# Kernel tuning notes

Hardware: AMD Instinct MI355X
Metric: run time of the kernel (lower is better)

Reference implementation:

```python
import jax, jax.numpy as jnp
import numpy as np

NUM_HEADS = 12
REDUCTION = 4
ALPHA_SPIKING = 0.5
ALPHA_ORIG = 0.5
K_BIAS = 1.0
BN_EPS = 1e-5


def dual_spike(x):
    # DualThresholdSelfregulatingIntegrateAction, T=1, dt=1: ternary spike at +/-1 thresholds
    return jnp.where(x >= 1.0, 1.0, jnp.where(x <= -1.0, -1.0, 0.0)).astype(x.dtype)


def setup_inputs() -> dict:
    key = jax.random.key(0)
    ks = jax.random.split(key, 12)
    B, S, Dm, H = 8, 512, 768, NUM_HEADS
    R = H // REDUCTION
    sc = 1.0 / np.sqrt(Dm).astype(np.float32)
    hidden_states = jax.random.normal(ks[0], (B, S, Dm), jnp.float32)
    attention_mask = jnp.zeros((B, 1, 1, S), jnp.float32)
    Wq = jax.random.normal(ks[1], (Dm, Dm), jnp.float32) * sc
    bq = jnp.zeros((Dm,), jnp.float32)
    Wk = jax.random.normal(ks[2], (Dm, Dm), jnp.float32) * sc
    bk = jnp.zeros((Dm,), jnp.float32)
    Wv = jax.random.normal(ks[3], (Dm, Dm), jnp.float32) * sc
    bv = jnp.zeros((Dm,), jnp.float32)
    # inline 1x1 convs of linesnn_mcz (bias=False), stored as [out_ch, in_ch]
    conv1_w = jax.random.normal(ks[4], (R, H), jnp.float32) * (1.0 / np.sqrt(H).astype(np.float32))
    bn_gamma = jnp.ones((R,), jnp.float32)
    bn_beta = jnp.zeros((R,), jnp.float32)
    convh_w = jax.random.normal(ks[5], (H, R), jnp.float32) * (1.0 / np.sqrt(R).astype(np.float32))
    convw_w = jax.random.normal(ks[6], (H, R), jnp.float32) * (1.0 / np.sqrt(R).astype(np.float32))
    return dict(hidden_states=hidden_states, attention_mask=attention_mask,
                Wq=Wq, bq=bq, Wk=Wk, bk=bk, Wv=Wv, bv=bv,
                conv1_w=conv1_w, bn_gamma=bn_gamma, bn_beta=bn_beta,
                convh_w=convh_w, convw_w=convw_w)


def _forward(hidden_states, attention_mask, Wq, bq, Wk, bk, Wv, bv,
             conv1_w, bn_gamma, bn_beta, convh_w, convw_w):
    B, S, Dm = hidden_states.shape
    H = NUM_HEADS
    D = Dm // H

    q_lin = hidden_states @ Wq + bq
    k_lin = hidden_states @ Wk + bk
    v_lin = jax.lax.stop_gradient(hidden_states @ Wv + bv)  # value is .detach()'d

    q = dual_spike(q_lin)                                   # spiking Q
    k = ALPHA_SPIKING * dual_spike(k_lin) + ALPHA_ORIG * k_lin

    def heads(x):  # [B,S,Dm] -> [B,H,S,D]
        return x.reshape(B, S, H, D).transpose(0, 2, 1, 3)

    q, k, v = heads(q), heads(k), heads(v_lin)

    scores = jnp.einsum('bhqd,bhkd->bhqk', q, k) / np.sqrt(D).astype(np.float32)

    # ---- select_linesnn / linesnn_mcz bias branch (on pre-mask scores) ----
    # spiking_activation_v then IF(v_th=1): spike = 1 where ternary spike == 1
    t = (dual_spike(scores) >= 1.0).astype(scores.dtype)    # [B,H,S,S]
    xh = t.mean(axis=3)                                     # mean over width  -> [B,H,S]
    xw = t.mean(axis=2)                                     # mean over height -> [B,H,S]
    cat = jnp.concatenate([xh, xw], axis=2)                 # [B,H,2S]
    y = jnp.einsum('rc,bcn->brn', conv1_w, cat)             # 1x1 conv H->R
    mu = y.mean(axis=(0, 2), keepdims=True)                 # BatchNorm (training stats)
    var = ((y - mu) ** 2).mean(axis=(0, 2), keepdims=True)
    y = (y - mu) * jax.lax.rsqrt(var + BN_EPS)
    y = y * bn_gamma[None, :, None] + bn_beta[None, :, None]
    y = jax.nn.relu(y)
    yh, yw = y[:, :, :S], y[:, :, S:]                       # split([h,w])
    s_h = jax.nn.sigmoid(jnp.einsum('hr,brs->bhs', convh_w, yh))  # [B,H,S]
    s_w = jax.nn.sigmoid(jnp.einsum('hr,brs->bhs', convw_w, yw))  # [B,H,S]
    bias = t * s_h[:, :, :, None] * s_w[:, :, None, :]      # [B,H,S,S]

    scores = scores + attention_mask + K_BIAS * bias
    probs = jax.nn.softmax(scores, axis=-1)                 # dropout p=0 (inference)
    ctx = jnp.einsum('bhqk,bhkd->bhqd', probs, v)
    return ctx.transpose(0, 2, 1, 3).reshape(B, S, Dm)


def reference(hidden_states, attention_mask, Wq, bq, Wk, bk, Wv, bv,
              conv1_w, bn_gamma, bn_beta, convh_w, convw_w):
    return _forward(hidden_states, attention_mask, Wq, bq, Wk, bk, Wv, bv,
                    conv1_w, bn_gamma, bn_beta, convh_w, convw_w)
```

## Files before the change

### kernel.cpp

```cpp
#include <hip/hip_runtime.h>
#include <math.h>

#define B_   8
#define S_   512
#define DM_  768
#define H_   12
#define D_   64
#define BH_  96
#define M_   4096

typedef _Float16 f16x8 __attribute__((ext_vector_type(8)));
typedef float    f32x4 __attribute__((ext_vector_type(4)));

__device__ __forceinline__ float dual_spike(float x) {
    return x >= 1.0f ? 1.0f : (x <= -1.0f ? -1.0f : 0.0f);
}

__device__ __forceinline__ void gload_lds16(const void* g, void* l) {
    __builtin_amdgcn_global_load_lds(
        (const __attribute__((address_space(1))) unsigned int*)g,
        (__attribute__((address_space(3))) unsigned int*)l, 16, 0, 0);
}

__device__ __forceinline__ f32x4 qk_dot(const f16x8* qa, const f16x8* kh, const f16x8* kl) {
    f32x4 acc = (f32x4){0.f, 0.f, 0.f, 0.f};
    acc = __builtin_amdgcn_mfma_f32_16x16x32_f16(qa[0], kh[0], acc, 0, 0, 0);
    acc = __builtin_amdgcn_mfma_f32_16x16x32_f16(qa[0], kl[0], acc, 0, 0, 0);
    acc = __builtin_amdgcn_mfma_f32_16x16x32_f16(qa[1], kh[1], acc, 0, 0, 0);
    acc = __builtin_amdgcn_mfma_f32_16x16x32_f16(qa[1], kl[1], acc, 0, 0, 0);
    return acc;
}

__global__ __launch_bounds__(256) void prep_x(
    const float* __restrict__ X, _Float16* __restrict__ Xh, _Float16* __restrict__ Xl)
{
    int wid  = blockIdx.x * 4 + (threadIdx.x >> 6);
    int lane = threadIdx.x & 63;
    int fm = wid & 255, kc = wid >> 8;
    int row = fm * 16 + (lane & 15);
    int col = kc * 32 + (lane >> 4) * 8;
    const float4* p = reinterpret_cast<const float4*>(&X[row * DM_ + col]);
    float4 x0 = p[0], x1 = p[1];
    float xs[8] = {x0.x, x0.y, x0.z, x0.w, x1.x, x1.y, x1.z, x1.w};
    f16x8 hi, lo;
    #pragma unroll
    for (int j = 0; j < 8; ++j) {
        float v = xs[j] * 256.0f;
        _Float16 h = (_Float16)v;
        hi[j] = h;
        lo[j] = (_Float16)(v - (float)h);
    }
    size_t out = ((size_t)wid * 64 + lane) * 8;
    *reinterpret_cast<f16x8*>(&Xh[out]) = hi;
    *reinterpret_cast<f16x8*>(&Xl[out]) = lo;
}

__global__ __launch_bounds__(256) void prep_w(
    const float* __restrict__ Wq, const float* __restrict__ Wk, const float* __restrict__ Wv,
    _Float16* __restrict__ Wth, _Float16* __restrict__ Wtl)
{
    int wid  = blockIdx.x * 4 + (threadIdx.x >> 6);
    int lane = threadIdx.x & 63;
    int fn = wid % 48, kc = (wid / 48) % 24, which = wid / 1152;
    const float* __restrict__ W = which == 0 ? Wq : (which == 1 ? Wk : Wv);
    int c = lane & 15, g = lane >> 4;
    int ncol = fn * 16 + c;
    int krow = kc * 32 + g * 8;
    f16x8 hi, lo;
    #pragma unroll
    for (int j = 0; j < 8; ++j) {
        float v = W[(krow + j) * DM_ + ncol] * 256.0f;
        _Float16 h = (_Float16)v;
        hi[j] = h;
        lo[j] = (_Float16)(v - (float)h);
    }
    size_t out = ((size_t)wid * 64 + lane) * 8;
    *reinterpret_cast<f16x8*>(&Wth[out]) = hi;
    *reinterpret_cast<f16x8*>(&Wtl[out]) = lo;
}

__global__ __launch_bounds__(512, 4) void qkv_mfma(
    const _Float16* __restrict__ Xh, const _Float16* __restrict__ Xl,
    const _Float16* __restrict__ Wth, const _Float16* __restrict__ Wtl,
    const float* __restrict__ X,
    const float* __restrict__ Wq, const float* __restrict__ bq,
    const float* __restrict__ Wk, const float* __restrict__ bk,
    const float* __restrict__ Wv, const float* __restrict__ bv,
    float* __restrict__ q, float* __restrict__ k, float* __restrict__ v)
{
    const int orig = blockIdx.x;
    const int xcd = orig & 7, idx = orig >> 3;
    const int epoch = idx >> 5, sub = idx & 31;
    const int mw = xcd * 12 + epoch * 4 + (sub >> 3);
    const int which = mw / 32, mb = mw % 32;
    const int nb = sub & 7;

    const float* __restrict__ bias = which == 0 ? bq : (which == 1 ? bk : bv);
    float* __restrict__ out        = which == 0 ? q  : (which == 1 ? k  : v);

    __shared__ __align__(16) _Float16 lds[2][14336];

    const int tid = threadIdx.x;
    const int wave = tid >> 6, lane = tid & 63;
    const int wm = wave >> 1, wn = wave & 1;
    const int l15 = lane & 15, g = lane >> 4;

    auto stage = [&](int kc, int bsel) {
        #pragma unroll
        for (int c = 0; c < 4; ++c) {
            int u = wave * 4 + c;
            if (u < 28) {
                const _Float16* src;
                if (u < 8)       src = Xh  + (size_t)(kc * 256 + mb * 8 + u) * 512;
                else if (u < 16) src = Xl  + (size_t)(kc * 256 + mb * 8 + (u - 8)) * 512;
                else if (u < 22) src = Wth + (size_t)((which * 24 + kc) * 48 + nb * 6 + (u - 16)) * 512;
                else             src = Wtl + (size_t)((which * 24 + kc) * 48 + nb * 6 + (u - 22)) * 512;
                gload_lds16(src + lane * 8, &lds[bsel][u * 512]);
            }
        }
    };

    f32x4 acc[2][3];
    #pragma unroll
    for (int i = 0; i < 2; ++i)
        #pragma unroll
        for (int j = 0; j < 3; ++j) acc[i][j] = (f32x4){0.f, 0.f, 0.f, 0.f};

    stage(0, 0);
    __syncthreads();
    int cur = 0;

    for (int kc = 0; kc < 24; ++kc) {
        if (kc + 1 < 24) stage(kc + 1, cur ^ 1);
        const _Float16* Bf = lds[cur];
        f16x8 ah[2], al[2], bh[3], bl[3];
        #pragma unroll
        for (int f = 0; f < 2; ++f) {
            ah[f] = *reinterpret_cast<const f16x8*>(&Bf[(wm * 2 + f) * 512 + lane * 8]);
            al[f] = *reinterpret_cast<const f16x8*>(&Bf[4096 + (wm * 2 + f) * 512 + lane * 8]);
        }
        #pragma unroll
        for (int fb = 0; fb < 3; ++fb) {
            bh[fb] = *reinterpret_cast<const f16x8*>(&Bf[8192 + (wn * 3 + fb) * 512 + lane * 8]);
            bl[fb] = *reinterpret_cast<const f16x8*>(&Bf[11264 + (wn * 3 + fb) * 512 + lane * 8]);
        }
        __builtin_amdgcn_s_setprio(1);
        #pragma unroll
        for (int i = 0; i < 2; ++i)
            #pragma unroll
            for (int j = 0; j < 3; ++j) {
                acc[i][j] = __builtin_amdgcn_mfma_f32_16x16x32_f16(ah[i], bh[j], acc[i][j], 0, 0, 0);
                acc[i][j] = __builtin_amdgcn_mfma_f32_16x16x32_f16(ah[i], bl[j], acc[i][j], 0, 0, 0);
                acc[i][j] = __builtin_amdgcn_mfma_f32_16x16x32_f16(al[i], bh[j], acc[i][j], 0, 0, 0);
            }
        __builtin_amdgcn_s_setprio(0);
        __syncthreads();
        cur ^= 1;
    }

    const float* __restrict__ Worig = which == 0 ? Wq : (which == 1 ? Wk : Wv);

    #pragma unroll
    for (int i = 0; i < 2; ++i) {
        #pragma unroll
        for (int j = 0; j < 3; ++j) {
            int n = nb * 96 + wn * 48 + j * 16 + l15;
            int h = n >> 6, d = n & 63;
            float bn = bias[n];
            #pragma unroll
            for (int r = 0; r < 4; ++r) {
                int m = mb * 128 + wm * 32 + i * 16 + g * 4 + r;
                float val = acc[i][j][r] * (1.0f / 65536.0f) + bn;
                if (which < 2) {
                    bool need = fabsf(fabsf(val) - 1.0f) < 1e-4f;
                    unsigned long long msk = __ballot(need);
                    while (msk) {
                        int L = (int)__builtin_ctzll(msk);
                        msk &= msk - 1;
                        int Lm = mb * 128 + wm * 32 + i * 16 + (L >> 4) * 4 + r;
                        int Ln = nb * 96 + wn * 48 + j * 16 + (L & 15);
                        const float* xr = X + (size_t)Lm * DM_;
                        const float* wc = Worig + Ln;
                        float xs[12], wsv[12];
                        #pragma unroll
                        for (int t = 0; t < 12; ++t) {
                            int e = t * 64 + lane;
                            xs[t]  = xr[e];
                            wsv[t] = wc[(size_t)e * DM_];
                        }
                        float part = 0.0f;
                        #pragma unroll
                        for (int t = 0; t < 12; ++t) part = fmaf(xs[t], wsv[t], part);
                        part += __shfl_xor(part, 1);
                        part += __shfl_xor(part, 2);
                        part += __shfl_xor(part, 4);
                        part += __shfl_xor(part, 8);
                        part += __shfl_xor(part, 16);
                        part += __shfl_xor(part, 32);
                        if (lane == L) val = part + bn;
                    }
                }
                if (which == 0)      val = dual_spike(val);
                else if (which == 1) val = 0.5f * dual_spike(val) + 0.5f * val;
                int b = m >> 9, s = m & 511;
                out[(((b * H_ + h) * S_) + s) * D_ + d] = val;
            }
        }
    }
}

__global__ __launch_bounds__(256) void prep_qkv(
    const float* __restrict__ q, const float* __restrict__ k, const float* __restrict__ v,
    _Float16* __restrict__ Qf, _Float16* __restrict__ Kfh, _Float16* __restrict__ Kfl,
    _Float16* __restrict__ Vfh, _Float16* __restrict__ Vfl)
{
    int lane = threadIdx.x & 63;
    int l15 = lane & 15, g = lane >> 4;
    if (blockIdx.x < 1536) {
        int wid  = blockIdx.x * 4 + (threadIdx.x >> 6);
        int dc = wid & 1, s16 = (wid >> 1) & 31, bh = wid >> 6;
        int s = s16 * 16 + l15;
        int d0 = dc * 32 + g * 8;
        const float* qp = &q[((size_t)bh * S_ + s) * D_ + d0];
        const float* kp = &k[((size_t)bh * S_ + s) * D_ + d0];
        f16x8 qv, kh, kl;
        #pragma unroll
        for (int j = 0; j < 8; ++j) {
            qv[j] = (_Float16)qp[j];
            float val = kp[j] * 256.0f;
            _Float16 h = (_Float16)val;
            kh[j] = h;
            kl[j] = (_Float16)(val - (float)h);
        }
        size_t o = (size_t)wid * 512 + lane * 8;
        *reinterpret_cast<f16x8*>(&Qf[o])  = qv;
        *reinterpret_cast<f16x8*>(&Kfh[o]) = kh;
        *reinterpret_cast<f16x8*>(&Kfl[o]) = kl;
    } else {
        int wid  = (blockIdx.x - 1536) * 4 + (threadIdx.x >> 6);
        int d16 = wid & 3, kc = (wid >> 2) & 15, bh = wid >> 6;
        int d = d16 * 16 + l15;
        int k0 = kc * 32 + g * 8;
        const float* vp = &v[((size_t)bh * S_ + k0) * D_ + d];
        f16x8 hi, lo;
        #pragma unroll
        for (int j = 0; j < 8; ++j) {
            float val = vp[j * D_];
            _Float16 h = (_Float16)val;
            hi[j] = h;
            lo[j] = (_Float16)(val - (float)h);
        }
        size_t o = (size_t)wid * 512 + lane * 8;
        *reinterpret_cast<f16x8*>(&Vfh[o]) = hi;
        *reinterpret_cast<f16x8*>(&Vfl[o]) = lo;
    }
}

__global__ __launch_bounds__(256) void score_sums(
    const _Float16* __restrict__ Qf, const _Float16* __restrict__ Kfh,
    const _Float16* __restrict__ Kfl,
    float* __restrict__ xh, float* __restrict__ xw)
{
    const int orig = blockIdx.x;
    const int xcd = orig & 7, idx = orig >> 3;
    const int bh = xcd * 12 + idx / 8, qt = idx & 7;
    const int tid = threadIdx.x, wave = tid >> 6, lane = tid & 63;
    const int l15 = lane & 15, g = lane >> 4;

    __shared__ float rowred[4][64];

    f16x8 qa[4][2];
    #pragma unroll
    for (int sf = 0; sf < 4; ++sf) {
        const _Float16* qb = Qf + (size_t)((bh * 32 + qt * 4 + sf) * 2) * 512 + lane * 8;
        qa[sf][0] = *reinterpret_cast<const f16x8*>(qb);
        qa[sf][1] = *reinterpret_cast<const f16x8*>(qb + 512);
    }
    float rowc[4][4];
    #pragma unroll
    for (int sf = 0; sf < 4; ++sf)
        #pragma unroll
        for (int r = 0; r < 4; ++r) rowc[sf][r] = 0.0f;

    for (int sc8 = 0; sc8 < 8; ++sc8) {
        int scol16 = sc8 * 4 + wave;
        const _Float16* kbh = Kfh + (size_t)((bh * 32 + scol16) * 2) * 512 + lane * 8;
        const _Float16* kbl = Kfl + (size_t)((bh * 32 + scol16) * 2) * 512 + lane * 8;
        f16x8 kh[2] = {*reinterpret_cast<const f16x8*>(kbh),
                       *reinterpret_cast<const f16x8*>(kbh + 512)};
        f16x8 kl[2] = {*reinterpret_cast<const f16x8*>(kbl),
                       *reinterpret_cast<const f16x8*>(kbl + 512)};
        float csum = 0.0f;
        #pragma unroll
        for (int sf = 0; sf < 4; ++sf) {
            f32x4 acc = qk_dot(qa[sf], kh, kl);
            #pragma unroll
            for (int r = 0; r < 4; ++r) {
                float t1 = acc[r] >= 2048.0f ? 1.0f : 0.0f;
                rowc[sf][r] += t1;
                csum += t1;
            }
        }
        csum += __shfl_xor(csum, 16);
        csum += __shfl_xor(csum, 32);
        if (g == 0) atomicAdd(&xw[bh * S_ + scol16 * 16 + l15], csum);
    }
    #pragma unroll
    for (int sf = 0; sf < 4; ++sf)
        #pragma unroll
        for (int r = 0; r < 4; ++r) {
            float sv = rowc[sf][r];
            sv += __shfl_xor(sv, 1); sv += __shfl_xor(sv, 2);
            sv += __shfl_xor(sv, 4); sv += __shfl_xor(sv, 8);
            if (l15 == 0) rowred[wave][sf * 16 + g * 4 + r] = sv;
        }
    __syncthreads();
    if (tid < 64) {
        float sv = rowred[0][tid] + rowred[1][tid] + rowred[2][tid] + rowred[3][tid];
        xh[bh * S_ + qt * 64 + tid] = sv;
    }
}

__global__ __launch_bounds__(256) void small_a(
    const float* __restrict__ xh, const float* __restrict__ xw,
    const float* __restrict__ c1w,
    float* __restrict__ y, float* __restrict__ stats_part)
{
    const int tid = threadIdx.x;
    const int br = blockIdx.x;
    const int r = br % 3, b = br / 3;
    __shared__ float c1s[12];
    __shared__ float red[256], red2[256];
    if (tid < 12) c1s[tid] = c1w[r * 12 + tid];
    __syncthreads();

    float psum = 0.0f, psq = 0.0f;
    for (int n = tid; n < 1024; n += 256) {
        float acc = 0.0f;
        #pragma unroll
        for (int h = 0; h < 12; ++h) {
            float cv = (n < 512) ? xh[(b * H_ + h) * S_ + n]
                                 : xw[(b * H_ + h) * S_ + (n - 512)];
            acc = fmaf(c1s[h], cv * (1.0f / 512.0f), acc);
        }
        y[br * 1024 + n] = acc;
        psum += acc;
        psq = fmaf(acc, acc, psq);
    }
    red[tid] = psum; red2[tid] = psq;
    __syncthreads();
    for (int o = 128; o > 0; o >>= 1) {
        if (tid < o) { red[tid] += red[tid + o]; red2[tid] += red2[tid + o]; }
        __syncthreads();
    }
    if (tid == 0) {
        stats_part[br * 2 + 0] = red[0];
        stats_part[br * 2 + 1] = red2[0];
    }
}

__global__ __launch_bounds__(512) void small_b(
    const float* __restrict__ y, const float* __restrict__ stats_part,
    const float* __restrict__ gamma, const float* __restrict__ beta,
    const float* __restrict__ chw, const float* __restrict__ cww,
    float* __restrict__ s_h, float* __restrict__ s_w)
{
    int e = blockIdx.x * 512 + threadIdx.x;
    int s = e & 511; int bh = e >> 9; int h = bh % H_; int b = bh / H_;
    float ah = 0.0f, aw = 0.0f;
    #pragma unroll
    for (int r = 0; r < 3; ++r) {
        float su = 0.0f, sq = 0.0f;
        #pragma unroll
        for (int bb = 0; bb < 8; ++bb) {
            su += stats_part[(bb * 3 + r) * 2 + 0];
            sq += stats_part[(bb * 3 + r) * 2 + 1];
        }
        float mu = su * (1.0f / 8192.0f);
        float var = sq * (1.0f / 8192.0f) - mu * mu;
        float rs = rsqrtf(var + 1e-5f);
        int yb = (b * 3 + r) << 10;
        float yh = fmaxf((y[yb + s]       - mu) * rs * gamma[r] + beta[r], 0.0f);
        float yw = fmaxf((y[yb + 512 + s] - mu) * rs * gamma[r] + beta[r], 0.0f);
        ah = fmaf(chw[h * 3 + r], yh, ah);
        aw = fmaf(cww[h * 3 + r], yw, aw);
    }
    s_h[e] = 1.0f / (1.0f + expf(-ah));
    s_w[e] = 1.0f / (1.0f + expf(-aw));
}

__global__ __launch_bounds__(256) void attn_pv(
    const _Float16* __restrict__ Qf, const _Float16* __restrict__ Kfh,
    const _Float16* __restrict__ Kfl,
    const _Float16* __restrict__ Vfh, const _Float16* __restrict__ Vfl,
    const float* __restrict__ mask, const float* __restrict__ s_h,
    const float* __restrict__ s_w, float* __restrict__ out)
{
    __shared__ __align__(16) _Float16 Kst[2][4096];
    __shared__ __align__(16) _Float16 Vst[2][4096];
    __shared__ __align__(16) float P_lds[64][68];

    const int orig = blockIdx.x;
    const int xcd = orig & 7, idx = orig >> 3;
    const int bh = xcd * 12 + idx / 8, qt = idx & 7;
    const int b = bh / H_, h = bh % H_;
    const int q0 = qt * 64;
    const int tid = threadIdx.x, wave = tid >> 6, lane = tid & 63;
    const int l15 = lane & 15, g = lane >> 4;
    const int rl = wave * 16 + g * 4;

    const _Float16* qb = Qf + (size_t)((bh * 32 + qt * 4 + wave) * 2) * 512 + lane * 8;
    f16x8 qa[2] = {*reinterpret_cast<const f16x8*>(qb),
                   *reinterpret_cast<const f16x8*>(qb + 512)};

    float shq[4];
    #pragma unroll
    for (int r = 0; r < 4; ++r) shq[r] = s_h[bh * S_ + q0 + rl + r];

    auto stageK = [&](int kt) {
        const _Float16* sh_ = Kfh + (size_t)((bh * 32 + kt * 4) * 2) * 512;
        const _Float16* sl_ = Kfl + (size_t)((bh * 32 + kt * 4) * 2) * 512;
        #pragma unroll
        for (int c = 0; c < 2; ++c) {
            int u = (c * 4 + wave) * 512;
            gload_lds16(&sh_[u + lane * 8], &Kst[0][u]);
            gload_lds16(&sl_[u + lane * 8], &Kst[1][u]);
        }
    };
    auto stageV = [&](int kt) {
        const _Float16* vh_ = Vfh + (size_t)((bh * 16 + kt * 2) * 4) * 512;
        const _Float16* vl_ = Vfl + (size_t)((bh * 16 + kt * 2) * 4) * 512;
        #pragma unroll
        for (int c = 0; c < 2; ++c) {
            int u = (c * 4 + wave) * 512;
            gload_lds16(&vh_[u + lane * 8], &Vst[0][u]);
            gload_lds16(&vl_[u + lane * 8], &Vst[1][u]);
        }
    };

    float m_r[4], l_r[4];
    f32x4 ctx[4];
    #pragma unroll
    for (int r = 0; r < 4; ++r) m_r[r] = -INFINITY, l_r[r] = 0.0f;
    #pragma unroll
    for (int fd = 0; fd < 4; ++fd) ctx[fd] = (f32x4){0.f, 0.f, 0.f, 0.f};

    stageK(0); stageV(0);
    __syncthreads();

    for (int kt = 0; kt < 8; ++kt) {
        float sc[4][4];
        __builtin_amdgcn_s_setprio(1);
        #pragma unroll
        for (int fc = 0; fc < 4; ++fc) {
            f16x8 kh[2] = {*reinterpret_cast<const f16x8*>(&Kst[0][(fc * 2 + 0) * 512 + lane * 8]),
                           *reinterpret_cast<const f16x8*>(&Kst[0][(fc * 2 + 1) * 512 + lane * 8])};
            f16x8 kl[2] = {*reinterpret_cast<const f16x8*>(&Kst[1][(fc * 2 + 0) * 512 + lane * 8]),
                           *reinterpret_cast<const f16x8*>(&Kst[1][(fc * 2 + 1) * 512 + lane * 8])};
            f32x4 acc = qk_dot(qa, kh, kl);
            int col = kt * 64 + fc * 16 + l15;
            float mj  = mask[b * S_ + col];
            float swj = s_w[bh * S_ + col];
            #pragma unroll
            for (int r = 0; r < 4; ++r) {
                float t1 = acc[r] >= 2048.0f ? 1.0f : 0.0f;
                sc[fc][r] = acc[r] * 4.8828125e-4f + mj + t1 * (shq[r] * swj);
            }
        }
        __builtin_amdgcn_s_setprio(0);
        __syncthreads();
        if (kt < 7) stageK(kt + 1);

        float p[4][4], cscale[4];
        #pragma unroll
        for (int r = 0; r < 4; ++r) {
            float tmax = fmaxf(fmaxf(sc[0][r], sc[1][r]), fmaxf(sc[2][r], sc[3][r]));
            tmax = fmaxf(tmax, __shfl_xor(tmax, 1));
            tmax = fmaxf(tmax, __shfl_xor(tmax, 2));
            tmax = fmaxf(tmax, __shfl_xor(tmax, 4));
            tmax = fmaxf(tmax, __shfl_xor(tmax, 8));
            float mn = fmaxf(m_r[r], tmax);
            float ps = 0.0f;
            #pragma unroll
            for (int fc = 0; fc < 4; ++fc) { p[fc][r] = expf(sc[fc][r] - mn); ps += p[fc][r]; }
            ps += __shfl_xor(ps, 1); ps += __shfl_xor(ps, 2);
            ps += __shfl_xor(ps, 4); ps += __shfl_xor(ps, 8);
            float scale = expf(m_r[r] - mn);
            l_r[r] = l_r[r] * scale + ps;
            m_r[r] = mn;
            cscale[r] = scale;
        }
        #pragma unroll
        for (int fc = 0; fc < 4; ++fc)
            #pragma unroll
            for (int r = 0; r < 4; ++r)
                P_lds[rl + r][fc * 16 + l15] = p[fc][r];

        f16x8 ph[2], pl[2];
        #pragma unroll
        for (int c = 0; c < 2; ++c) {
            f32x4 pa = *reinterpret_cast<const f32x4*>(&P_lds[wave * 16 + l15][c * 32 + g * 8]);
            f32x4 pb = *reinterpret_cast<const f32x4*>(&P_lds[wave * 16 + l15][c * 32 + g * 8 + 4]);
            float pv8[8] = {pa[0], pa[1], pa[2], pa[3], pb[0], pb[1], pb[2], pb[3]};
            #pragma unroll
            for (int j = 0; j < 8; ++j) {
                _Float16 hh = (_Float16)pv8[j];
                ph[c][j] = hh;
                pl[c][j] = (_Float16)(pv8[j] - (float)hh);
            }
        }
        #pragma unroll
        for (int fd = 0; fd < 4; ++fd)
            #pragma unroll
            for (int r = 0; r < 4; ++r) ctx[fd][r] *= cscale[r];

        __builtin_amdgcn_s_setprio(1);
        #pragma unroll
        for (int fd = 0; fd < 4; ++fd) {
            f16x8 vh0 = *reinterpret_cast<const f16x8*>(&Vst[0][(0 * 4 + fd) * 512 + lane * 8]);
            f16x8 vl0 = *reinterpret_cast<const f16x8*>(&Vst[1][(0 * 4 + fd) * 512 + lane * 8]);
            f16x8 vh1 = *reinterpret_cast<const f16x8*>(&Vst[0][(1 * 4 + fd) * 512 + lane * 8]);
            f16x8 vl1 = *reinterpret_cast<const f16x8*>(&Vst[1][(1 * 4 + fd) * 512 + lane * 8]);
            ctx[fd] = __builtin_amdgcn_mfma_f32_16x16x32_f16(ph[0], vh0, ctx[fd], 0, 0, 0);
            ctx[fd] = __builtin_amdgcn_mfma_f32_16x16x32_f16(ph[0], vl0, ctx[fd], 0, 0, 0);
            ctx[fd] = __builtin_amdgcn_mfma_f32_16x16x32_f16(pl[0], vh0, ctx[fd], 0, 0, 0);
            ctx[fd] = __builtin_amdgcn_mfma_f32_16x16x32_f16(ph[1], vh1, ctx[fd], 0, 0, 0);
            ctx[fd] = __builtin_amdgcn_mfma_f32_16x16x32_f16(ph[1], vl1, ctx[fd], 0, 0, 0);
            ctx[fd] = __builtin_amdgcn_mfma_f32_16x16x32_f16(pl[1], vh1, ctx[fd], 0, 0, 0);
        }
        __builtin_amdgcn_s_setprio(0);
        __syncthreads();
        if (kt < 7) stageV(kt + 1);
    }
    #pragma unroll
    for (int r = 0; r < 4; ++r) {
        int s = q0 + rl + r;
        float inv = 1.0f / l_r[r];
        float* orow = &out[((size_t)b * S_ + s) * DM_ + h * D_];
        #pragma unroll
        for (int fd = 0; fd < 4; ++fd)
            orow[fd * 16 + l15] = ctx[fd][r] * inv;
    }
}

extern "C" void kernel_launch(void* const* d_in, const int* in_sizes, int n_in,
                              void* d_out, int out_size, void* d_ws, size_t ws_size,
                              hipStream_t stream) {
    const float* X    = (const float*)d_in[0];
    const float* mask = (const float*)d_in[1];
    const float* Wq   = (const float*)d_in[2];
    const float* bq   = (const float*)d_in[3];
    const float* Wk   = (const float*)d_in[4];
    const float* bk   = (const float*)d_in[5];
    const float* Wv   = (const float*)d_in[6];
    const float* bv   = (const float*)d_in[7];
    const float* c1w  = (const float*)d_in[8];
    const float* gam  = (const float*)d_in[9];
    const float* bet  = (const float*)d_in[10];
    const float* chw  = (const float*)d_in[11];
    const float* cww  = (const float*)d_in[12];
    float* out = (float*)d_out;

    float* ws = (float*)d_ws;
    float* q  = ws;
    float* k  = q  + 3145728;
    float* v  = k  + 3145728;
    float* xh = v  + 3145728;
    float* xw = xh + 49152;
    float* y  = xw + 49152;
    float* sh = y  + 24576;
    float* sw = sh + 49152;
    _Float16* Xh  = (_Float16*)(sw + 49152);
    _Float16* Xl  = Xh + 3145728;
    _Float16* Wth = Xl + 3145728;
    _Float16* Wtl = Wth + 1769472;

    _Float16* Qf  = Xh;
    _Float16* Kfh = Xl;
    _Float16* Kfl = Wth;
    _Float16* Vfh = (_Float16*)k;
    _Float16* Vfl = Vfh + 3145728;
    float* stats_part = q;

    hipMemsetAsync(xw, 0, 49152 * sizeof(float), stream);

    prep_x<<<1536, 256, 0, stream>>>(X, Xh, Xl);
    prep_w<<<864, 256, 0, stream>>>(Wq, Wk, Wv, Wth, Wtl);
    qkv_mfma<<<768, 512, 0, stream>>>(Xh, Xl, Wth, Wtl,
        X, Wq, bq, Wk, bk, Wv, bv, q, k, v);
    prep_qkv<<<3072, 256, 0, stream>>>(q, k, v, Qf, Kfh, Kfl, Vfh, Vfl);
    score_sums<<<768, 256, 0, stream>>>(Qf, Kfh, Kfl, xh, xw);
    small_a<<<24, 256, 0, stream>>>(xh, xw, c1w, y, stats_part);
    small_b<<<96, 512, 0, stream>>>(y, stats_part, gam, bet, chw, cww, sh, sw);
    attn_pv<<<768, 256, 0, stream>>>(Qf, Kfh, Kfl, Vfh, Vfl, mask, sh, sw, out);
}
```

Measured before the change: 153.6 us.

## Fuse fp16 split and fragment-layout packing into QKV GEMM epilogue

The QKV GEMM epilogue now applies the spike transforms, splits values into hi/lo fp16 pairs, and writes them directly in the MFMA fragment layouts used by the attention kernels. This removes the separate prep_qkv kernel and the fp32 q/k/v round-trip through global memory. Workspace buffers are re-laid out to match. In exchange, the Q and K stores from the epilogue are scattered 2-byte writes that may coalesce poorly.

```diff
diff --git a/kernel.cpp b/kernel.cpp
--- a/kernel.cpp
+++ b/kernel.cpp
@@ -10,6 +10,7 @@
 #define M_   4096
 
 typedef _Float16 f16x8 __attribute__((ext_vector_type(8)));
+typedef _Float16 f16x4 __attribute__((ext_vector_type(4)));
 typedef float    f32x4 __attribute__((ext_vector_type(4)));
 
 __device__ __forceinline__ float dual_spike(float x) {
@@ -86,7 +87,8 @@
     const float* __restrict__ Wq, const float* __restrict__ bq,
     const float* __restrict__ Wk, const float* __restrict__ bk,
     const float* __restrict__ Wv, const float* __restrict__ bv,
-    float* __restrict__ q, float* __restrict__ k, float* __restrict__ v)
+    _Float16* __restrict__ Qf, _Float16* __restrict__ Kfh, _Float16* __restrict__ Kfl,
+    _Float16* __restrict__ Vfh, _Float16* __restrict__ Vfl)
 {
     const int orig = blockIdx.x;
     const int xcd = orig & 7, idx = orig >> 3;
@@ -96,7 +98,6 @@
     const int nb = sub & 7;
 
     const float* __restrict__ bias = which == 0 ? bq : (which == 1 ? bk : bv);
-    float* __restrict__ out        = which == 0 ? q  : (which == 1 ? k  : v);
 
     __shared__ __align__(16) _Float16 lds[2][14336];
 
@@ -167,9 +168,9 @@
             int n = nb * 96 + wn * 48 + j * 16 + l15;
             int h = n >> 6, d = n & 63;
             float bn = bias[n];
+            float vals[4];
             #pragma unroll
             for (int r = 0; r < 4; ++r) {
-                int m = mb * 128 + wm * 32 + i * 16 + g * 4 + r;
                 float val = acc[i][j][r] * (1.0f / 65536.0f) + bn;
                 if (which < 2) {
                     bool need = fabsf(fabsf(val) - 1.0f) < 1e-4f;
@@ -200,59 +201,45 @@
                         if (lane == L) val = part + bn;
                     }
                 }
-                if (which == 0)      val = dual_spike(val);
-                else if (which == 1) val = 0.5f * dual_spike(val) + 0.5f * val;
-                int b = m >> 9, s = m & 511;
-                out[(((b * H_ + h) * S_) + s) * D_ + d] = val;
-            }
-        }
-    }
-}
-
-__global__ __launch_bounds__(256) void prep_qkv(
-    const float* __restrict__ q, const float* __restrict__ k, const float* __restrict__ v,
-    _Float16* __restrict__ Qf, _Float16* __restrict__ Kfh, _Float16* __restrict__ Kfl,
-    _Float16* __restrict__ Vfh, _Float16* __restrict__ Vfl)
-{
-    int lane = threadIdx.x & 63;
-    int l15 = lane & 15, g = lane >> 4;
-    if (blockIdx.x < 1536) {
-        int wid  = blockIdx.x * 4 + (threadIdx.x >> 6);
-        int dc = wid & 1, s16 = (wid >> 1) & 31, bh = wid >> 6;
-        int s = s16 * 16 + l15;
-        int d0 = dc * 32 + g * 8;
-        const float* qp = &q[((size_t)bh * S_ + s) * D_ + d0];
-        const float* kp = &k[((size_t)bh * S_ + s) * D_ + d0];
-        f16x8 qv, kh, kl;
-        #pragma unroll
-        for (int j = 0; j < 8; ++j) {
-            qv[j] = (_Float16)qp[j];
-            float val = kp[j] * 256.0f;
-            _Float16 h = (_Float16)val;
-            kh[j] = h;
-            kl[j] = (_Float16)(val - (float)h);
-        }
-        size_t o = (size_t)wid * 512 + lane * 8;
-        *reinterpret_cast<f16x8*>(&Qf[o])  = qv;
-        *reinterpret_cast<f16x8*>(&Kfh[o]) = kh;
-        *reinterpret_cast<f16x8*>(&Kfl[o]) = kl;
-    } else {
-        int wid  = (blockIdx.x - 1536) * 4 + (threadIdx.x >> 6);
-        int d16 = wid & 3, kc = (wid >> 2) & 15, bh = wid >> 6;
-        int d = d16 * 16 + l15;
-        int k0 = kc * 32 + g * 8;
-        const float* vp = &v[((size_t)bh * S_ + k0) * D_ + d];
-        f16x8 hi, lo;
-        #pragma unroll
-        for (int j = 0; j < 8; ++j) {
-            float val = vp[j * D_];
-            _Float16 h = (_Float16)val;
-            hi[j] = h;
-            lo[j] = (_Float16)(val - (float)h);
-        }
-        size_t o = (size_t)wid * 512 + lane * 8;
-        *reinterpret_cast<f16x8*>(&Vfh[o]) = hi;
-        *reinterpret_cast<f16x8*>(&Vfl[o]) = lo;
+                vals[r] = val;
+            }
+            int m0 = mb * 128 + wm * 32 + i * 16 + g * 4;
+            int b = m0 >> 9, s0 = m0 & 511;
+            int bh_ = b * H_ + h;
+            if (which == 0) {
+                #pragma unroll
+                for (int r = 0; r < 4; ++r) {
+                    int s = s0 + r;
+                    size_t unit = (size_t)(bh_ * 32 + (s >> 4)) * 2 + (d >> 5);
+                    size_t off = unit * 512 + (size_t)(((d >> 3) & 3) * 16 + (s & 15)) * 8 + (d & 7);
+                    Qf[off] = (_Float16)dual_spike(vals[r]);
+                }
+            } else if (which == 1) {
+                #pragma unroll
+                for (int r = 0; r < 4; ++r) {
+                    int s = s0 + r;
+                    float kv = 0.5f * dual_spike(vals[r]) + 0.5f * vals[r];
+                    float sv = kv * 256.0f;
+                    _Float16 hh = (_Float16)sv;
+                    size_t unit = (size_t)(bh_ * 32 + (s >> 4)) * 2 + (d >> 5);
+                    size_t off = unit * 512 + (size_t)(((d >> 3) & 3) * 16 + (s & 15)) * 8 + (d & 7);
+                    Kfh[off] = hh;
+                    Kfl[off] = (_Float16)(sv - (float)hh);
+                }
+            } else {
+                f16x4 ph4, pl4;
+                #pragma unroll
+                for (int r = 0; r < 4; ++r) {
+                    _Float16 hh = (_Float16)vals[r];
+                    ph4[r] = hh;
+                    pl4[r] = (_Float16)(vals[r] - (float)hh);
+                }
+                size_t unit = (size_t)(bh_ * 16 + (s0 >> 5)) * 4 + (d >> 4);
+                size_t off = unit * 512 + (size_t)(((s0 >> 3) & 3) * 16 + (d & 15)) * 8 + (s0 & 7);
+                *reinterpret_cast<f16x4*>(&Vfh[off]) = ph4;
+                *reinterpret_cast<f16x4*>(&Vfl[off]) = pl4;
+            }
+        }
     }
 }
 
@@ -562,10 +549,13 @@
     float* out = (float*)d_out;
 
     float* ws = (float*)d_ws;
-    float* q  = ws;
-    float* k  = q  + 3145728;
-    float* v  = k  + 3145728;
-    float* xh = v  + 3145728;
+    _Float16* Qf  = (_Float16*)ws;
+    float* stats_part = (float*)(Qf + 3145728);
+    _Float16* Kfh = (_Float16*)(ws + 3145728);
+    _Float16* Kfl = Kfh + 3145728;
+    _Float16* Vfh = (_Float16*)(ws + 2 * 3145728);
+    _Float16* Vfl = Vfh + 3145728;
+    float* xh = ws + 3 * 3145728;
     float* xw = xh + 49152;
     float* y  = xw + 49152;
     float* sh = y  + 24576;
@@ -575,20 +565,12 @@
     _Float16* Wth = Xl + 3145728;
     _Float16* Wtl = Wth + 1769472;
 
-    _Float16* Qf  = Xh;
-    _Float16* Kfh = Xl;
-    _Float16* Kfl = Wth;
-    _Float16* Vfh = (_Float16*)k;
-    _Float16* Vfl = Vfh + 3145728;
-    float* stats_part = q;
-
     hipMemsetAsync(xw, 0, 49152 * sizeof(float), stream);
 
     prep_x<<<1536, 256, 0, stream>>>(X, Xh, Xl);
     prep_w<<<864, 256, 0, stream>>>(Wq, Wk, Wv, Wth, Wtl);
     qkv_mfma<<<768, 512, 0, stream>>>(Xh, Xl, Wth, Wtl,
-        X, Wq, bq, Wk, bk, Wv, bv, q, k, v);
-    prep_qkv<<<3072, 256, 0, stream>>>(q, k, v, Qf, Kfh, Kfl, Vfh, Vfl);
+        X, Wq, bq, Wk, bk, Wv, bv, Qf, Kfh, Kfl, Vfh, Vfl);
     score_sums<<<768, 256, 0, stream>>>(Qf, Kfh, Kfl, xh, xw);
     small_a<<<24, 256, 0, stream>>>(xh, xw, c1w, y, stats_part);
     small_b<<<96, 512, 0, stream>>>(y, stats_part, gam, bet, chw, cww, sh, sw);
```

Result: faster. 140.5 us (-8.6%).
